# Kernel tuning notes

Measured on AMD Instinct MI355X. Metric: run time of the kernel, lower is better.

## Reference

```python
import jax, jax.numpy as jnp
import numpy as np

MEMORY_SIZE = 32768
FEATURE_DIM = 128
BATCH = 4096


def setup_inputs() -> dict:
    key = jax.random.key(0)
    k1, k2, k3, k4 = jax.random.split(key, 4)
    memory = jax.random.normal(k1, (MEMORY_SIZE, FEATURE_DIM), dtype=jnp.float32)
    input_data = jax.random.normal(k2, (BATCH, FEATURE_DIM), dtype=jnp.float32)
    write_weights = jax.random.uniform(k3, (BATCH, MEMORY_SIZE), dtype=jnp.float32)
    query = jax.random.normal(k4, (BATCH, FEATURE_DIM), dtype=jnp.float32)
    return {"memory": memory, "input_data": input_data,
            "write_weights": write_weights, "query": query}


def reference(memory, input_data, write_weights, query):
    # ---- write(): row-normalize weights, scatter-accumulate into memory ----
    # The original python double-loop computes update[j] += w[i,j] * x[i],
    # i.e. update = w_norm.T @ x  -- a single GEMM.
    w_norm = write_weights / jnp.sum(write_weights, axis=1, keepdims=True)
    update = jnp.einsum('bm,bf->mf', w_norm, input_data)  # [M, F]
    memory_new = memory + update

    # ---- read(): softmax attention over memory slots ----
    scores = jnp.matmul(query, memory_new.T)              # [B, M]
    attention_weights = jax.nn.softmax(scores, axis=1)
    retrieved_memory = jnp.matmul(attention_weights, memory_new)  # [B, F]
    confidence_scores = jnp.max(attention_weights, axis=1)        # [B]
    return retrieved_memory, confidence_scores, memory_new
```

## Files before the change

kernel.cpp:

```cpp
#include <hip/hip_runtime.h>
#include <hip/hip_bf16.h>
#include <math.h>

#define MEMSZ 32768
#define FDIM  128
#define BATCH 4096

typedef float f32x4 __attribute__((ext_vector_type(4)));
typedef _Float16 f16x8 __attribute__((ext_vector_type(8)));
typedef short bf16x8 __attribute__((ext_vector_type(8)));
typedef unsigned short u16t;
typedef unsigned int u32t;

static __device__ __forceinline__ u16t f2h_bits(float f) {
    union { _Float16 h; u16t u; } c;
    c.h = (_Float16)f;
    return c.u;
}

#define GLDS16(gsrc, ldst) \
  __builtin_amdgcn_global_load_lds((const __attribute__((address_space(1))) void*)(gsrc), \
                                   (__attribute__((address_space(3))) void*)(ldst), 16, 0, 0)

__global__ __launch_bounds__(256) void k_rowsum(const float* __restrict__ W,
                                                float* __restrict__ inv_s) {
    const int row = blockIdx.x;
    const float4* Wr = reinterpret_cast<const float4*>(W + (size_t)row * MEMSZ);
    float acc = 0.f;
    #pragma unroll 4
    for (int i = threadIdx.x; i < MEMSZ / 4; i += 256) {
        float4 v = Wr[i];
        acc += (v.x + v.y) + (v.z + v.w);
    }
    #pragma unroll
    for (int off = 32; off > 0; off >>= 1)
        acc += __shfl_down(acc, off, 64);
    __shared__ float wsum[4];
    const int lane = threadIdx.x & 63, wid = threadIdx.x >> 6;
    if (lane == 0) wsum[wid] = acc;
    __syncthreads();
    if (threadIdx.x == 0)
        inv_s[row] = 1.0f / (wsum[0] + wsum[1] + wsum[2] + wsum[3]);
}

__global__ __launch_bounds__(256) void k_prep(const float* __restrict__ X,
                                              const float* __restrict__ inv_s,
                                              unsigned char* __restrict__ XT64) {
    __shared__ float xs[64][132];
    const int T = blockIdx.x;
    const int b0 = T * 64;
    const int tid = threadIdx.x;
    #pragma unroll
    for (int i = 0; i < 8; ++i) {
        const int idx = tid + i * 256;
        const int row = idx >> 5, c4 = idx & 31;
        const float s = inv_s[b0 + row];
        float4 v = *reinterpret_cast<const float4*>(&X[(size_t)(b0 + row) * FDIM + c4 * 4]);
        v.x *= s; v.y *= s; v.z *= s; v.w *= s;
        *reinterpret_cast<float4*>(&xs[row][c4 * 4]) = v;
    }
    __syncthreads();
    #pragma unroll
    for (int i = 0; i < 4; ++i) {
        const int L = tid + i * 256;
        const int fh = L >> 9, ff = (L >> 7) & 3, ks = (L >> 6) & 1, ln = L & 63;
        const int f = fh * 64 + ff * 16 + (ln & 15);
        const int bi = ks * 32 + (ln >> 4) * 8;
        u32t pk[4];
        #pragma unroll
        for (int h = 0; h < 4; ++h) {
            const float lo = xs[bi + 2 * h][f];
            const float hi = xs[bi + 2 * h + 1][f];
            asm("v_cvt_pk_bf16_f32 %0, %1, %2" : "=v"(pk[h]) : "v"(lo), "v"(hi));
        }
        *reinterpret_cast<uint4*>(XT64 + (size_t)T * 16384 + (size_t)L * 16) =
            make_uint4(pk[0], pk[1], pk[2], pk[3]);
    }
}

#define K2B 64
#define K2M 64
__global__ __launch_bounds__(256, 2) void k_update_mfma(
    const float* __restrict__ W, const unsigned char* __restrict__ XT64,
    const float* __restrict__ Mem, float* __restrict__ MemNew,
    u16t* __restrict__ MemH, u16t* __restrict__ MemHT)
{
    __shared__ __align__(16) unsigned char wt[2][16384];

    const int tid = threadIdx.x;
    const int lane = tid & 63, w = tid >> 6;
    const int q16 = lane & 15, g = lane >> 4;
    const int wm = w >> 1, wf = w & 1;
    const int mblk = blockIdx.x * K2M;

    f32x4 acc[2][4];
    #pragma unroll
    for (int mf = 0; mf < 2; ++mf)
        #pragma unroll
        for (int ff = 0; ff < 4; ++ff) acc[mf][ff] = (f32x4){0.f, 0.f, 0.f, 0.f};

    const unsigned char* xbase = XT64 + (size_t)(wf * 8192 + lane * 16);

    auto stageW = [&](int buf, int t) {
        const int b0 = t * K2B;
        #pragma unroll
        for (int c = 0; c < 4; ++c) {
            const int gi = c * 256 + tid;
            const int b = gi >> 4;
            const int src = ((gi & 15) * 16) ^ ((b & 8) << 1);
            GLDS16((const unsigned char*)W + (size_t)(b0 + b) * (MEMSZ * 4) + (size_t)mblk * 4 + src,
                   &wt[buf][gi * 16]);
        }
    };
    auto loadB = [&](bf16x8 (&br)[4][2], int t) {
        const unsigned char* xp = xbase + (size_t)t * 16384;
        #pragma unroll
        for (int ff = 0; ff < 4; ++ff)
            #pragma unroll
            for (int ks = 0; ks < 2; ++ks)
                br[ff][ks] = *reinterpret_cast<const bf16x8*>(xp + ff * 2048 + ks * 1024);
    };
    auto compute = [&](int buf, bf16x8 (&br)[4][2]) {
        bf16x8 afr[2][2];
        const unsigned char* tb = &wt[buf][0];
        #pragma unroll
        for (int mf = 0; mf < 2; ++mf) {
            const int mm4 = (wm * 32 + mf * 16 + q16) * 4;
            #pragma unroll
            for (int ks = 0; ks < 2; ++ks) {
                float av[8];
                #pragma unroll
                for (int e = 0; e < 8; ++e) {
                    const int b = ks * 32 + g * 8 + e;
                    av[e] = *reinterpret_cast<const float*>(
                        tb + b * 256 + (mm4 ^ ((b & 8) << 1)));
                }
                union { u32t u[4]; bf16x8 v; } cv;
                #pragma unroll
                for (int h = 0; h < 4; ++h)
                    asm("v_cvt_pk_bf16_f32 %0, %1, %2" : "=v"(cv.u[h]) : "v"(av[2 * h]), "v"(av[2 * h + 1]));
                afr[mf][ks] = cv.v;
            }
        }
        #pragma unroll
        for (int mf = 0; mf < 2; ++mf)
            #pragma unroll
            for (int ff = 0; ff < 4; ++ff)
                #pragma unroll
                for (int ks = 0; ks < 2; ++ks)
                    acc[mf][ff] = __builtin_amdgcn_mfma_f32_16x16x32_bf16(
                        afr[mf][ks], br[ff][ks], acc[mf][ff], 0, 0, 0);
    };

    bf16x8 bA[4][2], bB_[4][2];
    stageW(0, 0); loadB(bA, 0);
    const int NT = BATCH / K2B;
    for (int t = 0; t < NT; t += 2) {
        __builtin_amdgcn_s_barrier();
        if (t + 1 < NT) { loadB(bB_, t + 1); stageW(1, t + 1); }
        if (t + 1 < NT) asm volatile("s_waitcnt vmcnt(12)" ::: "memory");
        else            asm volatile("s_waitcnt vmcnt(0)"  ::: "memory");
        __builtin_amdgcn_s_barrier();
        __builtin_amdgcn_sched_barrier(0);
        compute(0, bA);
        __builtin_amdgcn_s_barrier();
        if (t + 2 < NT) { loadB(bA, t + 2); stageW(0, t + 2); }
        if (t + 2 < NT) asm volatile("s_waitcnt vmcnt(12)" ::: "memory");
        else            asm volatile("s_waitcnt vmcnt(0)"  ::: "memory");
        __builtin_amdgcn_s_barrier();
        __builtin_amdgcn_sched_barrier(0);
        compute(1, bB_);
    }

    #pragma unroll
    for (int mf = 0; mf < 2; ++mf) {
        #pragma unroll
        for (int ff = 0; ff < 4; ++ff) {
            const int m0 = mblk + wm * 32 + mf * 16 + g * 4;
            const int fcol = wf * 64 + ff * 16 + q16;
            ushort4 ht;
            u16t* htp = reinterpret_cast<u16t*>(&ht);
            #pragma unroll
            for (int r = 0; r < 4; ++r) {
                const size_t idx = (size_t)(m0 + r) * FDIM + fcol;
                const float v = acc[mf][ff][r] + Mem[idx];
                MemNew[idx] = v;
                const u16t hb = f2h_bits(v);
                MemH[idx] = hb;
                htp[r] = hb;
            }
            *reinterpret_cast<ushort4*>(&MemHT[(size_t)fcol * MEMSZ + m0]) = ht;
        }
    }
}

#define K2_IT 16
#define K2_MT 64
__global__ __launch_bounds__(256) void k_update_f32(const float* __restrict__ W,
                                                    const float* __restrict__ X,
                                                    const float* __restrict__ inv_s,
                                                    const float* __restrict__ Mem,
                                                    float* __restrict__ MemNew) {
    __shared__ float w_lds[2][K2_IT][K2_MT];
    __shared__ float x_lds[2][K2_IT][FDIM];
    const int j0 = blockIdx.x * K2_MT;
    const int tid = threadIdx.x;
    const int tf = tid & 15;
    const int tj = tid >> 4;

    float acc[4][8];
    #pragma unroll
    for (int a = 0; a < 4; ++a)
        #pragma unroll
        for (int b = 0; b < 8; ++b) acc[a][b] = 0.f;

    float4 pw, px0, px1;
    float ps0, ps1;
    const int wr = tid >> 4, wc4 = tid & 15;
    const int xr0 = tid >> 5, xc0 = tid & 31;
    const int xr1 = (tid + 256) >> 5, xc1 = tid & 31;

    auto load_tile = [&](int it) {
        const int i0 = it * K2_IT;
        pw  = *reinterpret_cast<const float4*>(&W[(size_t)(i0 + wr) * MEMSZ + j0 + wc4 * 4]);
        px0 = *reinterpret_cast<const float4*>(&X[(size_t)(i0 + xr0) * FDIM + xc0 * 4]);
        ps0 = inv_s[i0 + xr0];
        px1 = *reinterpret_cast<const float4*>(&X[(size_t)(i0 + xr1) * FDIM + xc1 * 4]);
        ps1 = inv_s[i0 + xr1];
    };
    auto write_tile = [&](int buf) {
        *reinterpret_cast<float4*>(&w_lds[buf][wr][wc4 * 4]) = pw;
        float4 v = px0; v.x *= ps0; v.y *= ps0; v.z *= ps0; v.w *= ps0;
        *reinterpret_cast<float4*>(&x_lds[buf][xr0][xc0 * 4]) = v;
        float4 u = px1; u.x *= ps1; u.y *= ps1; u.z *= ps1; u.w *= ps1;
        *reinterpret_cast<float4*>(&x_lds[buf][xr1][xc1 * 4]) = u;
    };

    load_tile(0);
    write_tile(0);
    __syncthreads();
    const int NT = BATCH / K2_IT;
    for (int it = 0; it < NT; ++it) {
        const int cur = it & 1;
        if (it + 1 < NT) load_tile(it + 1);
        #pragma unroll 4
        for (int i = 0; i < K2_IT; ++i) {
            const float4 wv = *reinterpret_cast<const float4*>(&w_lds[cur][i][tj * 4]);
            const float4 xa = *reinterpret_cast<const float4*>(&x_lds[cur][i][tf * 4]);
            const float4 xb = *reinterpret_cast<const float4*>(&x_lds[cur][i][tf * 4 + 64]);
            const float wj[4] = {wv.x, wv.y, wv.z, wv.w};
            #pragma unroll
            for (int a = 0; a < 4; ++a) {
                acc[a][0] += wj[a] * xa.x; acc[a][1] += wj[a] * xa.y;
                acc[a][2] += wj[a] * xa.z; acc[a][3] += wj[a] * xa.w;
                acc[a][4] += wj[a] * xb.x; acc[a][5] += wj[a] * xb.y;
                acc[a][6] += wj[a] * xb.z; acc[a][7] += wj[a] * xb.w;
            }
        }
        if (it + 1 < NT) write_tile(cur ^ 1);
        __syncthreads();
    }
    #pragma unroll
    for (int a = 0; a < 4; ++a) {
        const size_t j = (size_t)j0 + tj * 4 + a;
        const float4 m0 = *reinterpret_cast<const float4*>(&Mem[j * FDIM + tf * 4]);
        const float4 m1 = *reinterpret_cast<const float4*>(&Mem[j * FDIM + tf * 4 + 64]);
        float4 o0 = {acc[a][0] + m0.x, acc[a][1] + m0.y, acc[a][2] + m0.z, acc[a][3] + m0.w};
        float4 o1 = {acc[a][4] + m1.x, acc[a][5] + m1.y, acc[a][6] + m1.z, acc[a][7] + m1.w};
        *reinterpret_cast<float4*>(&MemNew[j * FDIM + tf * 4]) = o0;
        *reinterpret_cast<float4*>(&MemNew[j * FDIM + tf * 4 + 64]) = o1;
    }
}

__global__ __launch_bounds__(256) void k_attn_mfma(
    const float* __restrict__ Q, const u16t* __restrict__ Kh, const u16t* __restrict__ KhT,
    float* __restrict__ accP, float* __restrict__ mP, float* __restrict__ lP, int s_shift)
{
    __shared__ __align__(16) unsigned char kv_u8[2][16384];
    __shared__ __align__(16) unsigned char v_u8[2][16384];
    __shared__ __align__(16) unsigned char p_u8[4][2048];

    const int tid = threadIdx.x;
    const int w = tid >> 6, lane = tid & 63;
    const int q16 = lane & 15, g = lane >> 4;
    const int S = 1 << s_shift;
    const int s_idx = blockIdx.x & (S - 1);
    const int qb = blockIdx.x >> s_shift;
    const int chunk = MEMSZ >> s_shift;
    const int slot0 = s_idx * chunk;
    const int NT = chunk >> 6;

    f16x8 qfrag[2][4];
    #pragma unroll
    for (int qf = 0; qf < 2; ++qf) {
        const float* qrow = Q + (size_t)(qb * 128 + w * 32 + qf * 16 + q16) * FDIM;
        #pragma unroll
        for (int ks = 0; ks < 4; ++ks) {
            float tmp[8];
            *reinterpret_cast<float4*>(&tmp[0]) = *reinterpret_cast<const float4*>(&qrow[ks * 32 + g * 8]);
            *reinterpret_cast<float4*>(&tmp[4]) = *reinterpret_cast<const float4*>(&qrow[ks * 32 + g * 8 + 4]);
            f16x8 v;
            #pragma unroll
            for (int e = 0; e < 8; ++e) v[e] = (_Float16)tmp[e];
            qfrag[qf][ks] = v;
        }
    }

    auto stage = [&](int buf, int tile) {
        const unsigned char* kbase = (const unsigned char*)Kh + (size_t)(slot0 + tile * 64) * 256;
        const unsigned char* tbase = (const unsigned char*)KhT + (size_t)(slot0 + tile * 64) * 2;
        #pragma unroll
        for (int c = 0; c < 4; ++c) {
            const int C = w * 4 + c;
            const int pp = C * 1024 + lane * 16;
            {
                const int slot = pp >> 8;
                const int inner = (pp & 255) ^ ((slot & 7) << 4);
                GLDS16(kbase + slot * 256 + inner, &kv_u8[buf][C * 1024]);
            }
            {
                const int d = pp >> 7;
                const int inner = (pp & 127) ^ ((d & 7) << 4);
                GLDS16(tbase + (size_t)d * 65536 + inner, &v_u8[buf][C * 1024]);
            }
        }
    };

    float m_run[2] = {-3.0e38f, -3.0e38f};
    float l_run[2] = {0.f, 0.f};
    f32x4 acc_o[8][2];
    #pragma unroll
    for (int df = 0; df < 8; ++df)
        #pragma unroll
        for (int qf = 0; qf < 2; ++qf)
            acc_o[df][qf] = (f32x4){0.f, 0.f, 0.f, 0.f};

    stage(0, 0);
    asm volatile("s_waitcnt vmcnt(0)" ::: "memory");
    __builtin_amdgcn_s_barrier();
    __builtin_amdgcn_sched_barrier(0);

    int cur = 0;
    for (int t = 0; t < NT; ++t) {
        if (t + 1 < NT) stage(cur ^ 1, t + 1);

        f32x4 acc_s[4][2];
        #pragma unroll
        for (int sf = 0; sf < 4; ++sf) {
            acc_s[sf][0] = (f32x4){0.f, 0.f, 0.f, 0.f};
            acc_s[sf][1] = (f32x4){0.f, 0.f, 0.f, 0.f};
        }
        const unsigned char* kvb = &kv_u8[cur][0];
        #pragma unroll
        for (int ks = 0; ks < 4; ++ks) {
            #pragma unroll
            for (int sf = 0; sf < 4; ++sf) {
                const int slot = sf * 16 + q16;
                const f16x8 a = *reinterpret_cast<const f16x8*>(
                    kvb + slot * 256 + ((ks * 64 + g * 16) ^ ((slot & 7) << 4)));
                acc_s[sf][0] = __builtin_amdgcn_mfma_f32_16x16x32_f16(a, qfrag[0][ks], acc_s[sf][0], 0, 0, 0);
                acc_s[sf][1] = __builtin_amdgcn_mfma_f32_16x16x32_f16(a, qfrag[1][ks], acc_s[sf][1], 0, 0, 0);
            }
        }

        f16x8 pb[2][2];
        unsigned char* pw = &p_u8[w][0];
        #pragma unroll
        for (int qf = 0; qf < 2; ++qf) {
            float pmax = acc_s[0][qf][0];
            #pragma unroll
            for (int sf = 0; sf < 4; ++sf)
                #pragma unroll
                for (int r = 0; r < 4; ++r)
                    pmax = fmaxf(pmax, acc_s[sf][qf][r]);
            pmax = fmaxf(pmax, __shfl_xor(pmax, 16));
            pmax = fmaxf(pmax, __shfl_xor(pmax, 32));
            const float mn = fmaxf(m_run[qf], pmax);
            float p[4][4];
            float psum = 0.f;
            #pragma unroll
            for (int sf = 0; sf < 4; ++sf)
                #pragma unroll
                for (int r = 0; r < 4; ++r) {
                    p[sf][r] = __expf(acc_s[sf][qf][r] - mn);
                    psum += p[sf][r];
                }
            psum += __shfl_xor(psum, 16);
            psum += __shfl_xor(psum, 32);
            const float sc = __expf(m_run[qf] - mn);
            l_run[qf] = l_run[qf] * sc + psum;
            m_run[qf] = mn;
            #pragma unroll
            for (int df = 0; df < 8; ++df) {
                acc_o[df][qf][0] *= sc; acc_o[df][qf][1] *= sc;
                acc_o[df][qf][2] *= sc; acc_o[df][qf][3] *= sc;
            }
            #pragma unroll
            for (int sf = 0; sf < 4; ++sf)
                #pragma unroll
                for (int rr = 0; rr < 2; ++rr) {
                    const u32t val = (u32t)f2h_bits(p[sf][2 * rr]) | ((u32t)f2h_bits(p[sf][2 * rr + 1]) << 16);
                    const int byte = q16 * 128 + (((sf * 16 + g * 4 + 2 * rr) * 2) ^ ((q16 & 7) << 4));
                    *reinterpret_cast<u32t*>(pw + byte) = val;
                }
            #pragma unroll
            for (int kk = 0; kk < 2; ++kk) {
                const int byte = q16 * 128 + (((kk * 32 + g * 8) * 2) ^ ((q16 & 7) << 4));
                pb[qf][kk] = *reinterpret_cast<const f16x8*>(pw + byte);
            }
        }

        const unsigned char* vb = &v_u8[cur][0];
        #pragma unroll
        for (int df = 0; df < 8; ++df) {
            #pragma unroll
            for (int kk = 0; kk < 2; ++kk) {
                const int d = df * 16 + q16;
                const f16x8 av = *reinterpret_cast<const f16x8*>(
                    vb + d * 128 + ((kk * 64 + g * 16) ^ ((d & 7) << 4)));
                acc_o[df][0] = __builtin_amdgcn_mfma_f32_16x16x32_f16(av, pb[0][kk], acc_o[df][0], 0, 0, 0);
                acc_o[df][1] = __builtin_amdgcn_mfma_f32_16x16x32_f16(av, pb[1][kk], acc_o[df][1], 0, 0, 0);
            }
        }

        asm volatile("s_waitcnt vmcnt(0)" ::: "memory");
        __builtin_amdgcn_s_barrier();
        __builtin_amdgcn_sched_barrier(0);
        cur ^= 1;
    }

    const int rowbase = qb * 128 + w * 32;
    #pragma unroll
    for (int qf = 0; qf < 2; ++qf) {
        const int row = rowbase + qf * 16 + q16;
        float* ap = accP + ((size_t)s_idx * BATCH + row) * FDIM;
        #pragma unroll
        for (int df = 0; df < 8; ++df) {
            float4 o = {acc_o[df][qf][0], acc_o[df][qf][1], acc_o[df][qf][2], acc_o[df][qf][3]};
            *reinterpret_cast<float4*>(&ap[df * 16 + g * 4]) = o;
        }
        if (g == 0) {
            mP[(size_t)s_idx * BATCH + row] = m_run[qf];
            lP[(size_t)s_idx * BATCH + row] = l_run[qf];
        }
    }
}

__global__ __launch_bounds__(256) void k_combine(const float* __restrict__ mP,
                                                 const float* __restrict__ lP,
                                                 const float* __restrict__ accP,
                                                 float* __restrict__ Out,
                                                 float* __restrict__ Conf, int S) {
    const int row = blockIdx.x * 8 + (threadIdx.x >> 5);
    const int lane = threadIdx.x & 31;
    float mt = -3.0e38f;
    for (int s = 0; s < S; ++s) mt = fmaxf(mt, mP[(size_t)s * BATCH + row]);
    float lt = 0.f;
    for (int s = 0; s < S; ++s) lt += lP[(size_t)s * BATCH + row] * __expf(mP[(size_t)s * BATCH + row] - mt);
    const float inv = 1.0f / lt;
    float4 o = {0.f, 0.f, 0.f, 0.f};
    for (int s = 0; s < S; ++s) {
        const float wgt = __expf(mP[(size_t)s * BATCH + row] - mt);
        const float4 a = *reinterpret_cast<const float4*>(&accP[((size_t)s * BATCH + row) * FDIM + lane * 4]);
        o.x += wgt * a.x; o.y += wgt * a.y; o.z += wgt * a.z; o.w += wgt * a.w;
    }
    float4 res = {o.x * inv, o.y * inv, o.z * inv, o.w * inv};
    *reinterpret_cast<float4*>(&Out[(size_t)row * FDIM + lane * 4]) = res;
    if (lane == 0) Conf[row] = inv;
}

#define QT 16
#define MT 64
#define LSTR (FDIM + 4)
__global__ __launch_bounds__(256) void k_attn_f32(const float* __restrict__ Q,
                                                  const float* __restrict__ MemNew,
                                                  float* __restrict__ Out,
                                                  float* __restrict__ Conf) {
    __shared__ float mem_lds[MT][LSTR];
    __shared__ float q_lds[QT][LSTR];
    __shared__ float p_lds[QT][MT];
    __shared__ float m_lds[QT], l_lds[QT], scale_lds[QT];

    const int tid = threadIdx.x;
    const int qblk = blockIdx.x * QT;

    #pragma unroll
    for (int r = 0; r < 2; ++r) {
        const int idx = tid + r * 256;
        const int row = idx >> 5, c4 = idx & 31;
        *reinterpret_cast<float4*>(&q_lds[row][c4 * 4]) =
            *reinterpret_cast<const float4*>(&Q[(size_t)(qblk + row) * FDIM + c4 * 4]);
    }
    if (tid < QT) { m_lds[tid] = -3.0e38f; l_lds[tid] = 0.f; }

    const int sq = (tid >> 5) * 2;
    const int sm = tid & 31;
    const int pq = tid >> 4;
    const int pf = (tid & 15) * 4;

    float acc[8];
    #pragma unroll
    for (int e = 0; e < 8; ++e) acc[e] = 0.f;

    for (int mt = 0; mt < MEMSZ / MT; ++mt) {
        __syncthreads();
        const float* src = MemNew + (size_t)mt * MT * FDIM;
        #pragma unroll
        for (int r = 0; r < 8; ++r) {
            const int idx = tid + r * 256;
            const int row = idx >> 5, c4 = idx & 31;
            *reinterpret_cast<float4*>(&mem_lds[row][c4 * 4]) =
                *reinterpret_cast<const float4*>(&src[(size_t)row * FDIM + c4 * 4]);
        }
        const float mold0 = m_lds[sq], mold1 = m_lds[sq + 1];
        __syncthreads();

        float s00 = 0.f, s01 = 0.f, s10 = 0.f, s11 = 0.f;
        #pragma unroll 8
        for (int k = 0; k < FDIM; k += 4) {
            const float4 qa = *reinterpret_cast<const float4*>(&q_lds[sq][k]);
            const float4 qb = *reinterpret_cast<const float4*>(&q_lds[sq + 1][k]);
            const float4 ma = *reinterpret_cast<const float4*>(&mem_lds[sm][k]);
            const float4 mb = *reinterpret_cast<const float4*>(&mem_lds[sm + 32][k]);
            s00 += qa.x*ma.x + qa.y*ma.y + qa.z*ma.z + qa.w*ma.w;
            s01 += qa.x*mb.x + qa.y*mb.y + qa.z*mb.z + qa.w*mb.w;
            s10 += qb.x*ma.x + qb.y*ma.y + qb.z*ma.z + qb.w*ma.w;
            s11 += qb.x*mb.x + qb.y*mb.y + qb.z*mb.z + qb.w*mb.w;
        }
        float r0 = fmaxf(s00, s01), r1 = fmaxf(s10, s11);
        #pragma unroll
        for (int off = 1; off <= 16; off <<= 1) {
            r0 = fmaxf(r0, __shfl_xor(r0, off, 64));
            r1 = fmaxf(r1, __shfl_xor(r1, off, 64));
        }
        const float mn0 = fmaxf(mold0, r0), mn1 = fmaxf(mold1, r1);
        const float p00 = __expf(s00 - mn0), p01 = __expf(s01 - mn0);
        const float p10 = __expf(s10 - mn1), p11 = __expf(s11 - mn1);
        float t0 = p00 + p01, t1 = p10 + p11;
        #pragma unroll
        for (int off = 1; off <= 16; off <<= 1) {
            t0 += __shfl_xor(t0, off, 64);
            t1 += __shfl_xor(t1, off, 64);
        }
        p_lds[sq][sm]      = p00; p_lds[sq][sm + 32]     = p01;
        p_lds[sq + 1][sm]  = p10; p_lds[sq + 1][sm + 32] = p11;
        if (sm == 0) {
            const float sc0 = __expf(mold0 - mn0), sc1 = __expf(mold1 - mn1);
            m_lds[sq] = mn0; m_lds[sq + 1] = mn1;
            l_lds[sq]     = l_lds[sq]     * sc0 + t0;
            l_lds[sq + 1] = l_lds[sq + 1] * sc1 + t1;
            scale_lds[sq] = sc0; scale_lds[sq + 1] = sc1;
        }
        __syncthreads();

        const float sc = scale_lds[pq];
        #pragma unroll
        for (int e = 0; e < 8; ++e) acc[e] *= sc;
        #pragma unroll 8
        for (int m = 0; m < MT; ++m) {
            const float p = p_lds[pq][m];
            const float4 va = *reinterpret_cast<const float4*>(&mem_lds[m][pf]);
            const float4 vb = *reinterpret_cast<const float4*>(&mem_lds[m][pf + 64]);
            acc[0] += p * va.x; acc[1] += p * va.y; acc[2] += p * va.z; acc[3] += p * va.w;
            acc[4] += p * vb.x; acc[5] += p * vb.y; acc[6] += p * vb.z; acc[7] += p * vb.w;
        }
    }
    const float linv = 1.0f / l_lds[pq];
    float4 o0 = {acc[0]*linv, acc[1]*linv, acc[2]*linv, acc[3]*linv};
    float4 o1 = {acc[4]*linv, acc[5]*linv, acc[6]*linv, acc[7]*linv};
    *reinterpret_cast<float4*>(&Out[(size_t)(qblk + pq) * FDIM + pf]) = o0;
    *reinterpret_cast<float4*>(&Out[(size_t)(qblk + pq) * FDIM + pf + 64]) = o1;
    if (tid < QT) Conf[qblk + tid] = 1.0f / l_lds[tid];
}

extern "C" void kernel_launch(void* const* d_in, const int* in_sizes, int n_in,
                              void* d_out, int out_size, void* d_ws, size_t ws_size,
                              hipStream_t stream) {
    (void)in_sizes; (void)n_in; (void)out_size;
    const float* memory   = (const float*)d_in[0];
    const float* input    = (const float*)d_in[1];
    const float* wweights = (const float*)d_in[2];
    const float* query    = (const float*)d_in[3];

    float* out       = (float*)d_out;
    float* retrieved = out;
    float* conf      = out + (size_t)BATCH * FDIM;
    float* mem_new   = conf + BATCH;

    char* ws = (char*)d_ws;
    float* inv_s = (float*)ws;
    const size_t off_xt   = 16384;
    const size_t off_h    = off_xt + (size_t)FDIM * BATCH * 2;
    const size_t off_hT   = off_h + (size_t)MEMSZ * FDIM * 2;
    const size_t off_part = off_hT + (size_t)MEMSZ * FDIM * 2;

    int s_shift = -1;
    for (int sh = 4; sh >= 0; --sh) {
        const size_t S = (size_t)1 << sh;
        const size_t need = off_part + S * ((size_t)BATCH * 8 + (size_t)BATCH * FDIM * 4);
        if (ws_size >= need) { s_shift = sh; break; }
    }

    k_rowsum<<<BATCH, 256, 0, stream>>>(wweights, inv_s);
    if (s_shift >= 0) {
        const int S = 1 << s_shift;
        unsigned char* xt64 = (unsigned char*)(ws + off_xt);
        u16t* mh  = (u16t*)(ws + off_h);
        u16t* mhT = (u16t*)(ws + off_hT);
        float* mP   = (float*)(ws + off_part);
        float* lP   = mP + (size_t)S * BATCH;
        float* accP = lP + (size_t)S * BATCH;
        k_prep<<<BATCH / 64, 256, 0, stream>>>(input, inv_s, xt64);
        k_update_mfma<<<MEMSZ / K2M, 256, 0, stream>>>(wweights, xt64, memory, mem_new, mh, mhT);
        k_attn_mfma<<<(BATCH / 128) * S, 256, 0, stream>>>(query, mh, mhT, accP, mP, lP, s_shift);
        k_combine<<<BATCH / 8, 256, 0, stream>>>(mP, lP, accP, retrieved, conf, S);
    } else {
        k_update_f32<<<MEMSZ / K2_MT, 256, 0, stream>>>(wweights, input, inv_s, memory, mem_new);
        k_attn_f32<<<BATCH / QT, 256, 0, stream>>>(query, mem_new, retrieved, conf);
    }
}
```

Baseline: 399.3 us.

## Fuse update GEMM and attention into one persistent kernel with per-chunk flags

```diff
diff --git a/kernel.cpp b/kernel.cpp
--- a/kernel.cpp
+++ b/kernel.cpp
@@ -80,368 +80,303 @@
 
 #define K2B 64
 #define K2M 64
-__global__ __launch_bounds__(256, 2) void k_update_mfma(
+__global__ __launch_bounds__(256) void k_fused(
     const float* __restrict__ W, const unsigned char* __restrict__ XT64,
     const float* __restrict__ Mem, float* __restrict__ MemNew,
-    u16t* __restrict__ MemH, u16t* __restrict__ MemHT)
+    u16t* __restrict__ MemH, u16t* __restrict__ MemHT,
+    const float* __restrict__ Q,
+    float* __restrict__ accP, float* __restrict__ mP, float* __restrict__ lP,
+    int* __restrict__ flags)
 {
-    __shared__ __align__(16) unsigned char wt[2][16384];
-
+    __shared__ __align__(16) unsigned char smem[73728];
     const int tid = threadIdx.x;
     const int lane = tid & 63, w = tid >> 6;
     const int q16 = lane & 15, g = lane >> 4;
-    const int wm = w >> 1, wf = w & 1;
-    const int mblk = blockIdx.x * K2M;
-
-    f32x4 acc[2][4];
-    #pragma unroll
-    for (int mf = 0; mf < 2; ++mf)
-        #pragma unroll
-        for (int ff = 0; ff < 4; ++ff) acc[mf][ff] = (f32x4){0.f, 0.f, 0.f, 0.f};
-
-    const unsigned char* xbase = XT64 + (size_t)(wf * 8192 + lane * 16);
-
-    auto stageW = [&](int buf, int t) {
-        const int b0 = t * K2B;
-        #pragma unroll
-        for (int c = 0; c < 4; ++c) {
-            const int gi = c * 256 + tid;
-            const int b = gi >> 4;
-            const int src = ((gi & 15) * 16) ^ ((b & 8) << 1);
-            GLDS16((const unsigned char*)W + (size_t)(b0 + b) * (MEMSZ * 4) + (size_t)mblk * 4 + src,
-                   &wt[buf][gi * 16]);
-        }
-    };
-    auto loadB = [&](bf16x8 (&br)[4][2], int t) {
-        const unsigned char* xp = xbase + (size_t)t * 16384;
-        #pragma unroll
-        for (int ff = 0; ff < 4; ++ff)
-            #pragma unroll
-            for (int ks = 0; ks < 2; ++ks)
-                br[ff][ks] = *reinterpret_cast<const bf16x8*>(xp + ff * 2048 + ks * 1024);
-    };
-    auto compute = [&](int buf, bf16x8 (&br)[4][2]) {
-        bf16x8 afr[2][2];
-        const unsigned char* tb = &wt[buf][0];
+
+    if (blockIdx.x < 512) {
+        unsigned char* wt = smem;
+        const int wm = w >> 1, wf = w & 1;
+        const int mblk = blockIdx.x * K2M;
+
+        f32x4 acc[2][4];
+        #pragma unroll
+        for (int mf = 0; mf < 2; ++mf)
+            #pragma unroll
+            for (int ff = 0; ff < 4; ++ff) acc[mf][ff] = (f32x4){0.f, 0.f, 0.f, 0.f};
+
+        const unsigned char* xbase = XT64 + (size_t)(wf * 8192 + lane * 16);
+
+        auto stageW = [&](int buf, int t) {
+            const int b0 = t * K2B;
+            #pragma unroll
+            for (int c = 0; c < 4; ++c) {
+                const int gi = c * 256 + tid;
+                const int b = gi >> 4;
+                const int src = ((gi & 15) * 16) ^ ((b & 8) << 1);
+                GLDS16((const unsigned char*)W + (size_t)(b0 + b) * (MEMSZ * 4) + (size_t)mblk * 4 + src,
+                       wt + buf * 16384 + gi * 16);
+            }
+        };
+        auto loadB = [&](bf16x8 (&br)[4][2], int t) {
+            const unsigned char* xp = xbase + (size_t)t * 16384;
+            #pragma unroll
+            for (int ff = 0; ff < 4; ++ff)
+                #pragma unroll
+                for (int ks = 0; ks < 2; ++ks)
+                    br[ff][ks] = *reinterpret_cast<const bf16x8*>(xp + ff * 2048 + ks * 1024);
+        };
+        auto compute = [&](int buf, bf16x8 (&br)[4][2]) {
+            bf16x8 afr[2][2];
+            const unsigned char* tb = wt + buf * 16384;
+            #pragma unroll
+            for (int mf = 0; mf < 2; ++mf) {
+                const int mm4 = (wm * 32 + mf * 16 + q16) * 4;
+                #pragma unroll
+                for (int ks = 0; ks < 2; ++ks) {
+                    float av[8];
+                    #pragma unroll
+                    for (int e = 0; e < 8; ++e) {
+                        const int b = ks * 32 + g * 8 + e;
+                        av[e] = *reinterpret_cast<const float*>(
+                            tb + b * 256 + (mm4 ^ ((b & 8) << 1)));
+                    }
+                    union { u32t u[4]; bf16x8 v; } cv;
+                    #pragma unroll
+                    for (int h = 0; h < 4; ++h)
+                        asm("v_cvt_pk_bf16_f32 %0, %1, %2" : "=v"(cv.u[h]) : "v"(av[2 * h]), "v"(av[2 * h + 1]));
+                    afr[mf][ks] = cv.v;
+                }
+            }
+            #pragma unroll
+            for (int mf = 0; mf < 2; ++mf)
+                #pragma unroll
+                for (int ff = 0; ff < 4; ++ff)
+                    #pragma unroll
+                    for (int ks = 0; ks < 2; ++ks)
+                        acc[mf][ff] = __builtin_amdgcn_mfma_f32_16x16x32_bf16(
+                            afr[mf][ks], br[ff][ks], acc[mf][ff], 0, 0, 0);
+        };
+
+        bf16x8 bA[4][2], bB_[4][2];
+        stageW(0, 0); loadB(bA, 0);
+        const int NT = BATCH / K2B;
+        for (int t = 0; t < NT; t += 2) {
+            __builtin_amdgcn_s_barrier();
+            if (t + 1 < NT) { loadB(bB_, t + 1); stageW(1, t + 1); }
+            if (t + 1 < NT) asm volatile("s_waitcnt vmcnt(12)" ::: "memory");
+            else            asm volatile("s_waitcnt vmcnt(0)"  ::: "memory");
+            __builtin_amdgcn_s_barrier();
+            __builtin_amdgcn_sched_barrier(0);
+            compute(0, bA);
+            __builtin_amdgcn_s_barrier();
+            if (t + 2 < NT) { loadB(bA, t + 2); stageW(0, t + 2); }
+            if (t + 2 < NT) asm volatile("s_waitcnt vmcnt(12)" ::: "memory");
+            else            asm volatile("s_waitcnt vmcnt(0)"  ::: "memory");
+            __builtin_amdgcn_s_barrier();
+            __builtin_amdgcn_sched_barrier(0);
+            compute(1, bB_);
+        }
+
         #pragma unroll
         for (int mf = 0; mf < 2; ++mf) {
-            const int mm4 = (wm * 32 + mf * 16 + q16) * 4;
-            #pragma unroll
-            for (int ks = 0; ks < 2; ++ks) {
-                float av[8];
-                #pragma unroll
-                for (int e = 0; e < 8; ++e) {
-                    const int b = ks * 32 + g * 8 + e;
-                    av[e] = *reinterpret_cast<const float*>(
-                        tb + b * 256 + (mm4 ^ ((b & 8) << 1)));
-                }
-                union { u32t u[4]; bf16x8 v; } cv;
-                #pragma unroll
-                for (int h = 0; h < 4; ++h)
-                    asm("v_cvt_pk_bf16_f32 %0, %1, %2" : "=v"(cv.u[h]) : "v"(av[2 * h]), "v"(av[2 * h + 1]));
-                afr[mf][ks] = cv.v;
-            }
-        }
-        #pragma unroll
-        for (int mf = 0; mf < 2; ++mf)
-            #pragma unroll
-            for (int ff = 0; ff < 4; ++ff)
-                #pragma unroll
-                for (int ks = 0; ks < 2; ++ks)
-                    acc[mf][ff] = __builtin_amdgcn_mfma_f32_16x16x32_bf16(
-                        afr[mf][ks], br[ff][ks], acc[mf][ff], 0, 0, 0);
-    };
-
-    bf16x8 bA[4][2], bB_[4][2];
-    stageW(0, 0); loadB(bA, 0);
-    const int NT = BATCH / K2B;
-    for (int t = 0; t < NT; t += 2) {
-        __builtin_amdgcn_s_barrier();
-        if (t + 1 < NT) { loadB(bB_, t + 1); stageW(1, t + 1); }
-        if (t + 1 < NT) asm volatile("s_waitcnt vmcnt(12)" ::: "memory");
-        else            asm volatile("s_waitcnt vmcnt(0)"  ::: "memory");
-        __builtin_amdgcn_s_barrier();
-        __builtin_amdgcn_sched_barrier(0);
-        compute(0, bA);
-        __builtin_amdgcn_s_barrier();
-        if (t + 2 < NT) { loadB(bA, t + 2); stageW(0, t + 2); }
-        if (t + 2 < NT) asm volatile("s_waitcnt vmcnt(12)" ::: "memory");
-        else            asm volatile("s_waitcnt vmcnt(0)"  ::: "memory");
-        __builtin_amdgcn_s_barrier();
-        __builtin_amdgcn_sched_barrier(0);
-        compute(1, bB_);
-    }
-
-    #pragma unroll
-    for (int mf = 0; mf < 2; ++mf) {
-        #pragma unroll
-        for (int ff = 0; ff < 4; ++ff) {
-            const int m0 = mblk + wm * 32 + mf * 16 + g * 4;
-            const int fcol = wf * 64 + ff * 16 + q16;
-            ushort4 ht;
-            u16t* htp = reinterpret_cast<u16t*>(&ht);
-            #pragma unroll
-            for (int r = 0; r < 4; ++r) {
-                const size_t idx = (size_t)(m0 + r) * FDIM + fcol;
-                const float v = acc[mf][ff][r] + Mem[idx];
-                MemNew[idx] = v;
-                const u16t hb = f2h_bits(v);
-                MemH[idx] = hb;
-                htp[r] = hb;
-            }
-            *reinterpret_cast<ushort4*>(&MemHT[(size_t)fcol * MEMSZ + m0]) = ht;
-        }
-    }
-}
-
-#define K2_IT 16
-#define K2_MT 64
-__global__ __launch_bounds__(256) void k_update_f32(const float* __restrict__ W,
-                                                    const float* __restrict__ X,
-                                                    const float* __restrict__ inv_s,
-                                                    const float* __restrict__ Mem,
-                                                    float* __restrict__ MemNew) {
-    __shared__ float w_lds[2][K2_IT][K2_MT];
-    __shared__ float x_lds[2][K2_IT][FDIM];
-    const int j0 = blockIdx.x * K2_MT;
-    const int tid = threadIdx.x;
-    const int tf = tid & 15;
-    const int tj = tid >> 4;
-
-    float acc[4][8];
-    #pragma unroll
-    for (int a = 0; a < 4; ++a)
-        #pragma unroll
-        for (int b = 0; b < 8; ++b) acc[a][b] = 0.f;
-
-    float4 pw, px0, px1;
-    float ps0, ps1;
-    const int wr = tid >> 4, wc4 = tid & 15;
-    const int xr0 = tid >> 5, xc0 = tid & 31;
-    const int xr1 = (tid + 256) >> 5, xc1 = tid & 31;
-
-    auto load_tile = [&](int it) {
-        const int i0 = it * K2_IT;
-        pw  = *reinterpret_cast<const float4*>(&W[(size_t)(i0 + wr) * MEMSZ + j0 + wc4 * 4]);
-        px0 = *reinterpret_cast<const float4*>(&X[(size_t)(i0 + xr0) * FDIM + xc0 * 4]);
-        ps0 = inv_s[i0 + xr0];
-        px1 = *reinterpret_cast<const float4*>(&X[(size_t)(i0 + xr1) * FDIM + xc1 * 4]);
-        ps1 = inv_s[i0 + xr1];
-    };
-    auto write_tile = [&](int buf) {
-        *reinterpret_cast<float4*>(&w_lds[buf][wr][wc4 * 4]) = pw;
-        float4 v = px0; v.x *= ps0; v.y *= ps0; v.z *= ps0; v.w *= ps0;
-        *reinterpret_cast<float4*>(&x_lds[buf][xr0][xc0 * 4]) = v;
-        float4 u = px1; u.x *= ps1; u.y *= ps1; u.z *= ps1; u.w *= ps1;
-        *reinterpret_cast<float4*>(&x_lds[buf][xr1][xc1 * 4]) = u;
-    };
-
-    load_tile(0);
-    write_tile(0);
-    __syncthreads();
-    const int NT = BATCH / K2_IT;
-    for (int it = 0; it < NT; ++it) {
-        const int cur = it & 1;
-        if (it + 1 < NT) load_tile(it + 1);
-        #pragma unroll 4
-        for (int i = 0; i < K2_IT; ++i) {
-            const float4 wv = *reinterpret_cast<const float4*>(&w_lds[cur][i][tj * 4]);
-            const float4 xa = *reinterpret_cast<const float4*>(&x_lds[cur][i][tf * 4]);
-            const float4 xb = *reinterpret_cast<const float4*>(&x_lds[cur][i][tf * 4 + 64]);
-            const float wj[4] = {wv.x, wv.y, wv.z, wv.w};
-            #pragma unroll
-            for (int a = 0; a < 4; ++a) {
-                acc[a][0] += wj[a] * xa.x; acc[a][1] += wj[a] * xa.y;
-                acc[a][2] += wj[a] * xa.z; acc[a][3] += wj[a] * xa.w;
-                acc[a][4] += wj[a] * xb.x; acc[a][5] += wj[a] * xb.y;
-                acc[a][6] += wj[a] * xb.z; acc[a][7] += wj[a] * xb.w;
-            }
-        }
-        if (it + 1 < NT) write_tile(cur ^ 1);
+            #pragma unroll
+            for (int ff = 0; ff < 4; ++ff) {
+                const int m0 = mblk + wm * 32 + mf * 16 + g * 4;
+                const int fcol = wf * 64 + ff * 16 + q16;
+                ushort4 ht;
+                u16t* htp = reinterpret_cast<u16t*>(&ht);
+                #pragma unroll
+                for (int r = 0; r < 4; ++r) {
+                    const size_t idx = (size_t)(m0 + r) * FDIM + fcol;
+                    const float v = acc[mf][ff][r] + Mem[idx];
+                    MemNew[idx] = v;
+                    const u16t hb = f2h_bits(v);
+                    MemH[idx] = hb;
+                    htp[r] = hb;
+                }
+                *reinterpret_cast<ushort4*>(&MemHT[(size_t)fcol * MEMSZ + m0]) = ht;
+            }
+        }
         __syncthreads();
-    }
-    #pragma unroll
-    for (int a = 0; a < 4; ++a) {
-        const size_t j = (size_t)j0 + tj * 4 + a;
-        const float4 m0 = *reinterpret_cast<const float4*>(&Mem[j * FDIM + tf * 4]);
-        const float4 m1 = *reinterpret_cast<const float4*>(&Mem[j * FDIM + tf * 4 + 64]);
-        float4 o0 = {acc[a][0] + m0.x, acc[a][1] + m0.y, acc[a][2] + m0.z, acc[a][3] + m0.w};
-        float4 o1 = {acc[a][4] + m1.x, acc[a][5] + m1.y, acc[a][6] + m1.z, acc[a][7] + m1.w};
-        *reinterpret_cast<float4*>(&MemNew[j * FDIM + tf * 4]) = o0;
-        *reinterpret_cast<float4*>(&MemNew[j * FDIM + tf * 4 + 64]) = o1;
-    }
-}
-
-__global__ __launch_bounds__(256) void k_attn_mfma(
-    const float* __restrict__ Q, const u16t* __restrict__ Kh, const u16t* __restrict__ KhT,
-    float* __restrict__ accP, float* __restrict__ mP, float* __restrict__ lP, int s_shift)
-{
-    __shared__ __align__(16) unsigned char kv_u8[2][16384];
-    __shared__ __align__(16) unsigned char v_u8[2][16384];
-    __shared__ __align__(16) unsigned char p_u8[4][2048];
-
-    const int tid = threadIdx.x;
-    const int w = tid >> 6, lane = tid & 63;
-    const int q16 = lane & 15, g = lane >> 4;
-    const int S = 1 << s_shift;
-    const int s_idx = blockIdx.x & (S - 1);
-    const int qb = blockIdx.x >> s_shift;
-    const int chunk = MEMSZ >> s_shift;
-    const int slot0 = s_idx * chunk;
-    const int NT = chunk >> 6;
-
-    f16x8 qfrag[2][4];
-    #pragma unroll
-    for (int qf = 0; qf < 2; ++qf) {
-        const float* qrow = Q + (size_t)(qb * 128 + w * 32 + qf * 16 + q16) * FDIM;
-        #pragma unroll
-        for (int ks = 0; ks < 4; ++ks) {
-            float tmp[8];
-            *reinterpret_cast<float4*>(&tmp[0]) = *reinterpret_cast<const float4*>(&qrow[ks * 32 + g * 8]);
-            *reinterpret_cast<float4*>(&tmp[4]) = *reinterpret_cast<const float4*>(&qrow[ks * 32 + g * 8 + 4]);
-            f16x8 v;
-            #pragma unroll
-            for (int e = 0; e < 8; ++e) v[e] = (_Float16)tmp[e];
-            qfrag[qf][ks] = v;
-        }
-    }
-
-    auto stage = [&](int buf, int tile) {
-        const unsigned char* kbase = (const unsigned char*)Kh + (size_t)(slot0 + tile * 64) * 256;
-        const unsigned char* tbase = (const unsigned char*)KhT + (size_t)(slot0 + tile * 64) * 2;
-        #pragma unroll
-        for (int c = 0; c < 4; ++c) {
-            const int C = w * 4 + c;
-            const int pp = C * 1024 + lane * 16;
-            {
-                const int slot = pp >> 8;
-                const int inner = (pp & 255) ^ ((slot & 7) << 4);
-                GLDS16(kbase + slot * 256 + inner, &kv_u8[buf][C * 1024]);
-            }
-            {
-                const int d = pp >> 7;
-                const int inner = (pp & 127) ^ ((d & 7) << 4);
-                GLDS16(tbase + (size_t)d * 65536 + inner, &v_u8[buf][C * 1024]);
-            }
-        }
-    };
-
-    float m_run[2] = {-3.0e38f, -3.0e38f};
-    float l_run[2] = {0.f, 0.f};
-    f32x4 acc_o[8][2];
-    #pragma unroll
-    for (int df = 0; df < 8; ++df)
-        #pragma unroll
-        for (int qf = 0; qf < 2; ++qf)
-            acc_o[df][qf] = (f32x4){0.f, 0.f, 0.f, 0.f};
-
-    stage(0, 0);
-    asm volatile("s_waitcnt vmcnt(0)" ::: "memory");
-    __builtin_amdgcn_s_barrier();
-    __builtin_amdgcn_sched_barrier(0);
-
-    int cur = 0;
-    for (int t = 0; t < NT; ++t) {
-        if (t + 1 < NT) stage(cur ^ 1, t + 1);
-
-        f32x4 acc_s[4][2];
-        #pragma unroll
-        for (int sf = 0; sf < 4; ++sf) {
-            acc_s[sf][0] = (f32x4){0.f, 0.f, 0.f, 0.f};
-            acc_s[sf][1] = (f32x4){0.f, 0.f, 0.f, 0.f};
-        }
-        const unsigned char* kvb = &kv_u8[cur][0];
-        #pragma unroll
-        for (int ks = 0; ks < 4; ++ks) {
-            #pragma unroll
-            for (int sf = 0; sf < 4; ++sf) {
-                const int slot = sf * 16 + q16;
-                const f16x8 a = *reinterpret_cast<const f16x8*>(
-                    kvb + slot * 256 + ((ks * 64 + g * 16) ^ ((slot & 7) << 4)));
-                acc_s[sf][0] = __builtin_amdgcn_mfma_f32_16x16x32_f16(a, qfrag[0][ks], acc_s[sf][0], 0, 0, 0);
-                acc_s[sf][1] = __builtin_amdgcn_mfma_f32_16x16x32_f16(a, qfrag[1][ks], acc_s[sf][1], 0, 0, 0);
-            }
-        }
-
-        f16x8 pb[2][2];
-        unsigned char* pw = &p_u8[w][0];
+        if (tid == 0) {
+            __threadfence();
+            atomicAdd(&flags[blockIdx.x >> 5], 1);
+        }
+    } else {
+        const int i = blockIdx.x - 512;
+        const int s_idx = i >> 5;
+        const int qb = i & 31;
+        const int slot0 = s_idx * 2048;
+        const int NT = 32;
+
+        unsigned char* kv_u8 = smem;
+        unsigned char* v_u8  = smem + 32768;
+        unsigned char* p_u8  = smem + 65536;
+
+        if (tid == 0) {
+            while (atomicAdd(&flags[s_idx], 0) < 32)
+                __builtin_amdgcn_s_sleep(32);
+        }
+        __syncthreads();
+        __threadfence();
+
+        f16x8 qfrag[2][4];
         #pragma unroll
         for (int qf = 0; qf < 2; ++qf) {
-            float pmax = acc_s[0][qf][0];
-            #pragma unroll
-            for (int sf = 0; sf < 4; ++sf)
-                #pragma unroll
-                for (int r = 0; r < 4; ++r)
-                    pmax = fmaxf(pmax, acc_s[sf][qf][r]);
-            pmax = fmaxf(pmax, __shfl_xor(pmax, 16));
-            pmax = fmaxf(pmax, __shfl_xor(pmax, 32));
-            const float mn = fmaxf(m_run[qf], pmax);
-            float p[4][4];
-            float psum = 0.f;
-            #pragma unroll
-            for (int sf = 0; sf < 4; ++sf)
-                #pragma unroll
-                for (int r = 0; r < 4; ++r) {
-                    p[sf][r] = __expf(acc_s[sf][qf][r] - mn);
-                    psum += p[sf][r];
-                }
-            psum += __shfl_xor(psum, 16);
-            psum += __shfl_xor(psum, 32);
-            const float sc = __expf(m_run[qf] - mn);
-            l_run[qf] = l_run[qf] * sc + psum;
-            m_run[qf] = mn;
-            #pragma unroll
-            for (int df = 0; df < 8; ++df) {
-                acc_o[df][qf][0] *= sc; acc_o[df][qf][1] *= sc;
-                acc_o[df][qf][2] *= sc; acc_o[df][qf][3] *= sc;
-            }
-            #pragma unroll
-            for (int sf = 0; sf < 4; ++sf)
-                #pragma unroll
-                for (int rr = 0; rr < 2; ++rr) {
-                    const u32t val = (u32t)f2h_bits(p[sf][2 * rr]) | ((u32t)f2h_bits(p[sf][2 * rr + 1]) << 16);
-                    const int byte = q16 * 128 + (((sf * 16 + g * 4 + 2 * rr) * 2) ^ ((q16 & 7) << 4));
-                    *reinterpret_cast<u32t*>(pw + byte) = val;
-                }
-            #pragma unroll
-            for (int kk = 0; kk < 2; ++kk) {
-                const int byte = q16 * 128 + (((kk * 32 + g * 8) * 2) ^ ((q16 & 7) << 4));
-                pb[qf][kk] = *reinterpret_cast<const f16x8*>(pw + byte);
-            }
-        }
-
-        const unsigned char* vb = &v_u8[cur][0];
-        #pragma unroll
-        for (int df = 0; df < 8; ++df) {
-            #pragma unroll
-            for (int kk = 0; kk < 2; ++kk) {
-                const int d = df * 16 + q16;
-                const f16x8 av = *reinterpret_cast<const f16x8*>(
-                    vb + d * 128 + ((kk * 64 + g * 16) ^ ((d & 7) << 4)));
-                acc_o[df][0] = __builtin_amdgcn_mfma_f32_16x16x32_f16(av, pb[0][kk], acc_o[df][0], 0, 0, 0);
-                acc_o[df][1] = __builtin_amdgcn_mfma_f32_16x16x32_f16(av, pb[1][kk], acc_o[df][1], 0, 0, 0);
-            }
-        }
-
+            const float* qrow = Q + (size_t)(qb * 128 + w * 32 + qf * 16 + q16) * FDIM;
+            #pragma unroll
+            for (int ks = 0; ks < 4; ++ks) {
+                float tmp[8];
+                *reinterpret_cast<float4*>(&tmp[0]) = *reinterpret_cast<const float4*>(&qrow[ks * 32 + g * 8]);
+                *reinterpret_cast<float4*>(&tmp[4]) = *reinterpret_cast<const float4*>(&qrow[ks * 32 + g * 8 + 4]);
+                f16x8 v;
+                #pragma unroll
+                for (int e = 0; e < 8; ++e) v[e] = (_Float16)tmp[e];
+                qfrag[qf][ks] = v;
+            }
+        }
+
+        auto stage = [&](int buf, int tile) {
+            const unsigned char* kbase = (const unsigned char*)MemH + (size_t)(slot0 + tile * 64) * 256;
+            const unsigned char* tbase = (const unsigned char*)MemHT + (size_t)(slot0 + tile * 64) * 2;
+            #pragma unroll
+            for (int c = 0; c < 4; ++c) {
+                const int C = w * 4 + c;
+                const int pp = C * 1024 + lane * 16;
+                {
+                    const int slot = pp >> 8;
+                    const int inner = (pp & 255) ^ ((slot & 7) << 4);
+                    GLDS16(kbase + slot * 256 + inner, kv_u8 + buf * 16384 + C * 1024);
+                }
+                {
+                    const int d = pp >> 7;
+                    const int inner = (pp & 127) ^ ((d & 7) << 4);
+                    GLDS16(tbase + (size_t)d * 65536 + inner, v_u8 + buf * 16384 + C * 1024);
+                }
+            }
+        };
+
+        float m_run[2] = {-3.0e38f, -3.0e38f};
+        float l_run[2] = {0.f, 0.f};
+        f32x4 acc_o[8][2];
+        #pragma unroll
+        for (int df = 0; df < 8; ++df)
+            #pragma unroll
+            for (int qf = 0; qf < 2; ++qf)
+                acc_o[df][qf] = (f32x4){0.f, 0.f, 0.f, 0.f};
+
+        stage(0, 0);
         asm volatile("s_waitcnt vmcnt(0)" ::: "memory");
         __builtin_amdgcn_s_barrier();
         __builtin_amdgcn_sched_barrier(0);
-        cur ^= 1;
-    }
-
-    const int rowbase = qb * 128 + w * 32;
-    #pragma unroll
-    for (int qf = 0; qf < 2; ++qf) {
-        const int row = rowbase + qf * 16 + q16;
-        float* ap = accP + ((size_t)s_idx * BATCH + row) * FDIM;
-        #pragma unroll
-        for (int df = 0; df < 8; ++df) {
-            float4 o = {acc_o[df][qf][0], acc_o[df][qf][1], acc_o[df][qf][2], acc_o[df][qf][3]};
-            *reinterpret_cast<float4*>(&ap[df * 16 + g * 4]) = o;
-        }
-        if (g == 0) {
-            mP[(size_t)s_idx * BATCH + row] = m_run[qf];
-            lP[(size_t)s_idx * BATCH + row] = l_run[qf];
+
+        int cur = 0;
+        for (int t = 0; t < NT; ++t) {
+            if (t + 1 < NT) stage(cur ^ 1, t + 1);
+
+            f32x4 acc_s[4][2];
+            #pragma unroll
+            for (int sf = 0; sf < 4; ++sf) {
+                acc_s[sf][0] = (f32x4){0.f, 0.f, 0.f, 0.f};
+                acc_s[sf][1] = (f32x4){0.f, 0.f, 0.f, 0.f};
+            }
+            const unsigned char* kvb = kv_u8 + cur * 16384;
+            __builtin_amdgcn_s_setprio(1);
+            #pragma unroll
+            for (int ks = 0; ks < 4; ++ks) {
+                #pragma unroll
+                for (int sf = 0; sf < 4; ++sf) {
+                    const int slot = sf * 16 + q16;
+                    const f16x8 a = *reinterpret_cast<const f16x8*>(
+                        kvb + slot * 256 + ((ks * 64 + g * 16) ^ ((slot & 7) << 4)));
+                    acc_s[sf][0] = __builtin_amdgcn_mfma_f32_16x16x32_f16(a, qfrag[0][ks], acc_s[sf][0], 0, 0, 0);
+                    acc_s[sf][1] = __builtin_amdgcn_mfma_f32_16x16x32_f16(a, qfrag[1][ks], acc_s[sf][1], 0, 0, 0);
+                }
+            }
+            __builtin_amdgcn_s_setprio(0);
+
+            f16x8 pb[2][2];
+            unsigned char* pw = p_u8 + w * 2048;
+            #pragma unroll
+            for (int qf = 0; qf < 2; ++qf) {
+                float pmax = acc_s[0][qf][0];
+                #pragma unroll
+                for (int sf = 0; sf < 4; ++sf)
+                    #pragma unroll
+                    for (int r = 0; r < 4; ++r)
+                        pmax = fmaxf(pmax, acc_s[sf][qf][r]);
+                pmax = fmaxf(pmax, __shfl_xor(pmax, 16));
+                pmax = fmaxf(pmax, __shfl_xor(pmax, 32));
+                const float mn = fmaxf(m_run[qf], pmax);
+                float p[4][4];
+                float psum = 0.f;
+                #pragma unroll
+                for (int sf = 0; sf < 4; ++sf)
+                    #pragma unroll
+                    for (int r = 0; r < 4; ++r) {
+                        p[sf][r] = __expf(acc_s[sf][qf][r] - mn);
+                        psum += p[sf][r];
+                    }
+                psum += __shfl_xor(psum, 16);
+                psum += __shfl_xor(psum, 32);
+                const float sc = __expf(m_run[qf] - mn);
+                l_run[qf] = l_run[qf] * sc + psum;
+                m_run[qf] = mn;
+                #pragma unroll
+                for (int df = 0; df < 8; ++df) {
+                    acc_o[df][qf][0] *= sc; acc_o[df][qf][1] *= sc;
+                    acc_o[df][qf][2] *= sc; acc_o[df][qf][3] *= sc;
+                }
+                #pragma unroll
+                for (int sf = 0; sf < 4; ++sf)
+                    #pragma unroll
+                    for (int rr = 0; rr < 2; ++rr) {
+                        const u32t val = (u32t)f2h_bits(p[sf][2 * rr]) | ((u32t)f2h_bits(p[sf][2 * rr + 1]) << 16);
+                        const int byte = q16 * 128 + (((sf * 16 + g * 4 + 2 * rr) * 2) ^ ((q16 & 7) << 4));
+                        *reinterpret_cast<u32t*>(pw + byte) = val;
+                    }
+                #pragma unroll
+                for (int kk = 0; kk < 2; ++kk) {
+                    const int byte = q16 * 128 + (((kk * 32 + g * 8) * 2) ^ ((q16 & 7) << 4));
+                    pb[qf][kk] = *reinterpret_cast<const f16x8*>(pw + byte);
+                }
+            }
+
+            const unsigned char* vb = v_u8 + cur * 16384;
+            __builtin_amdgcn_s_setprio(1);
+            #pragma unroll
+            for (int df = 0; df < 8; ++df) {
+                #pragma unroll
+                for (int kk = 0; kk < 2; ++kk) {
+                    const int d = df * 16 + q16;
+                    const f16x8 av = *reinterpret_cast<const f16x8*>(
+                        vb + d * 128 + ((kk * 64 + g * 16) ^ ((d & 7) << 4)));
+                    acc_o[df][0] = __builtin_amdgcn_mfma_f32_16x16x32_f16(av, pb[0][kk], acc_o[df][0], 0, 0, 0);
+                    acc_o[df][1] = __builtin_amdgcn_mfma_f32_16x16x32_f16(av, pb[1][kk], acc_o[df][1], 0, 0, 0);
+                }
+            }
+            __builtin_amdgcn_s_setprio(0);
+
+            asm volatile("s_waitcnt vmcnt(0)" ::: "memory");
+            __builtin_amdgcn_s_barrier();
+            __builtin_amdgcn_sched_barrier(0);
+            cur ^= 1;
+        }
+
+        const int rowbase = qb * 128 + w * 32;
+        #pragma unroll
+        for (int qf = 0; qf < 2; ++qf) {
+            const int row = rowbase + qf * 16 + q16;
+            float* ap = accP + ((size_t)s_idx * BATCH + row) * FDIM;
+            #pragma unroll
+            for (int df = 0; df < 8; ++df) {
+                float4 o = {acc_o[df][qf][0], acc_o[df][qf][1], acc_o[df][qf][2], acc_o[df][qf][3]};
+                *reinterpret_cast<float4*>(&ap[df * 16 + g * 4]) = o;
+            }
+            if (g == 0) {
+                mP[(size_t)s_idx * BATCH + row] = m_run[qf];
+                lP[(size_t)s_idx * BATCH + row] = l_run[qf];
+            }
         }
     }
 }
@@ -469,6 +404,84 @@
     if (lane == 0) Conf[row] = inv;
 }
 
+#define K2_IT 16
+#define K2_MT 64
+__global__ __launch_bounds__(256) void k_update_f32(const float* __restrict__ W,
+                                                    const float* __restrict__ X,
+                                                    const float* __restrict__ inv_s,
+                                                    const float* __restrict__ Mem,
+                                                    float* __restrict__ MemNew) {
+    __shared__ float w_lds[2][K2_IT][K2_MT];
+    __shared__ float x_lds[2][K2_IT][FDIM];
+    const int j0 = blockIdx.x * K2_MT;
+    const int tid = threadIdx.x;
+    const int tf = tid & 15;
+    const int tj = tid >> 4;
+
+    float acc[4][8];
+    #pragma unroll
+    for (int a = 0; a < 4; ++a)
+        #pragma unroll
+        for (int b = 0; b < 8; ++b) acc[a][b] = 0.f;
+
+    float4 pw, px0, px1;
+    float ps0, ps1;
+    const int wr = tid >> 4, wc4 = tid & 15;
+    const int xr0 = tid >> 5, xc0 = tid & 31;
+    const int xr1 = (tid + 256) >> 5, xc1 = tid & 31;
+
+    auto load_tile = [&](int it) {
+        const int i0 = it * K2_IT;
+        pw  = *reinterpret_cast<const float4*>(&W[(size_t)(i0 + wr) * MEMSZ + j0 + wc4 * 4]);
+        px0 = *reinterpret_cast<const float4*>(&X[(size_t)(i0 + xr0) * FDIM + xc0 * 4]);
+        ps0 = inv_s[i0 + xr0];
+        px1 = *reinterpret_cast<const float4*>(&X[(size_t)(i0 + xr1) * FDIM + xc1 * 4]);
+        ps1 = inv_s[i0 + xr1];
+    };
+    auto write_tile = [&](int buf) {
+        *reinterpret_cast<float4*>(&w_lds[buf][wr][wc4 * 4]) = pw;
+        float4 v = px0; v.x *= ps0; v.y *= ps0; v.z *= ps0; v.w *= ps0;
+        *reinterpret_cast<float4*>(&x_lds[buf][xr0][xc0 * 4]) = v;
+        float4 u = px1; u.x *= ps1; u.y *= ps1; u.z *= ps1; u.w *= ps1;
+        *reinterpret_cast<float4*>(&x_lds[buf][xr1][xc1 * 4]) = u;
+    };
+
+    load_tile(0);
+    write_tile(0);
+    __syncthreads();
+    const int NT = BATCH / K2_IT;
+    for (int it = 0; it < NT; ++it) {
+        const int cur = it & 1;
+        if (it + 1 < NT) load_tile(it + 1);
+        #pragma unroll 4
+        for (int i = 0; i < K2_IT; ++i) {
+            const float4 wv = *reinterpret_cast<const float4*>(&w_lds[cur][i][tj * 4]);
+            const float4 xa = *reinterpret_cast<const float4*>(&x_lds[cur][i][tf * 4]);
+            const float4 xb = *reinterpret_cast<const float4*>(&x_lds[cur][i][tf * 4 + 64]);
+            const float wj[4] = {wv.x, wv.y, wv.z, wv.w};
+            #pragma unroll
+            for (int a = 0; a < 4; ++a) {
+                acc[a][0] += wj[a] * xa.x; acc[a][1] += wj[a] * xa.y;
+                acc[a][2] += wj[a] * xa.z; acc[a][3] += wj[a] * xa.w;
+                acc[a][4] += wj[a] * xb.x; acc[a][5] += wj[a] * xb.y;
+                acc[a][6] += wj[a] * xb.z; acc[a][7] += wj[a] * xb.w;
+            }
+        }
+        if (it + 1 < NT) write_tile(cur ^ 1);
+        __syncthreads();
+    }
+    #pragma unroll
+    for (int a = 0; a < 4; ++a) {
+        const size_t j = (size_t)j0 + tj * 4 + a;
+        const float4 m0 = *reinterpret_cast<const float4*>(&Mem[j * FDIM + tf * 4]);
+        const float4 m1 = *reinterpret_cast<const float4*>(&Mem[j * FDIM + tf * 4 + 64]);
+        float4 o0 = {acc[a][0] + m0.x, acc[a][1] + m0.y, acc[a][2] + m0.z, acc[a][3] + m0.w};
+        float4 o1 = {acc[a][4] + m1.x, acc[a][5] + m1.y, acc[a][6] + m1.z, acc[a][7] + m1.w};
+        *reinterpret_cast<float4*>(&MemNew[j * FDIM + tf * 4]) = o0;
+        *reinterpret_cast<float4*>(&MemNew[j * FDIM + tf * 4 + 64]) = o1;
+    }
+}
+
 #define QT 16
 #define MT 64
 #define LSTR (FDIM + 4)
@@ -589,31 +602,29 @@
 
     char* ws = (char*)d_ws;
     float* inv_s = (float*)ws;
-    const size_t off_xt   = 16384;
-    const size_t off_h    = off_xt + (size_t)FDIM * BATCH * 2;
-    const size_t off_hT   = off_h + (size_t)MEMSZ * FDIM * 2;
-    const size_t off_part = off_hT + (size_t)MEMSZ * FDIM * 2;
-
-    int s_shift = -1;
-    for (int sh = 4; sh >= 0; --sh) {
-        const size_t S = (size_t)1 << sh;
-        const size_t need = off_part + S * ((size_t)BATCH * 8 + (size_t)BATCH * FDIM * 4);
-        if (ws_size >= need) { s_shift = sh; break; }
-    }
+    const size_t off_flags = 16384;
+    const size_t off_xt    = off_flags + 512;
+    const size_t off_h     = off_xt + (size_t)FDIM * BATCH * 2;
+    const size_t off_hT    = off_h + (size_t)MEMSZ * FDIM * 2;
+    const size_t off_part  = off_hT + (size_t)MEMSZ * FDIM * 2;
+    const size_t need_full = off_part + (size_t)16 * ((size_t)BATCH * 8 + (size_t)BATCH * FDIM * 4);
 
     k_rowsum<<<BATCH, 256, 0, stream>>>(wweights, inv_s);
-    if (s_shift >= 0) {
-        const int S = 1 << s_shift;
+
+    if (ws_size >= need_full) {
+        int* flags = (int*)(ws + off_flags);
         unsigned char* xt64 = (unsigned char*)(ws + off_xt);
         u16t* mh  = (u16t*)(ws + off_h);
         u16t* mhT = (u16t*)(ws + off_hT);
         float* mP   = (float*)(ws + off_part);
-        float* lP   = mP + (size_t)S * BATCH;
-        float* accP = lP + (size_t)S * BATCH;
+        float* lP   = mP + (size_t)16 * BATCH;
+        float* accP = lP + (size_t)16 * BATCH;
+
+        hipMemsetAsync((void*)flags, 0, 64, stream);
         k_prep<<<BATCH / 64, 256, 0, stream>>>(input, inv_s, xt64);
-        k_update_mfma<<<MEMSZ / K2M, 256, 0, stream>>>(wweights, xt64, memory, mem_new, mh, mhT);
-        k_attn_mfma<<<(BATCH / 128) * S, 256, 0, stream>>>(query, mh, mhT, accP, mP, lP, s_shift);
-        k_combine<<<BATCH / 8, 256, 0, stream>>>(mP, lP, accP, retrieved, conf, S);
+        k_fused<<<1024, 256, 0, stream>>>(wweights, xt64, memory, mem_new, mh, mhT,
+                                          query, accP, mP, lP, flags);
+        k_combine<<<BATCH / 8, 256, 0, stream>>>(mP, lP, accP, retrieved, conf, 16);
     } else {
         k_update_f32<<<MEMSZ / K2_MT, 256, 0, stream>>>(wweights, input, inv_s, memory, mem_new);
         k_attn_f32<<<BATCH / QT, 256, 0, stream>>>(query, mem_new, retrieved, conf);
```

After: 479.4 us. 20.0% more time.
